# Kernel optimization log

Measured on AMD Instinct MI355X. Metric: run time of the kernel, lower is better.

Reference implementation:

```python
import jax, jax.numpy as jnp
import numpy as np


def setup_inputs() -> dict:
    key = jax.random.key(0)
    kx, ke = jax.random.split(key)
    B, D, H, W, K = 64, 64, 32, 32, 512
    x = jax.random.normal(kx, (B, D, H, W), dtype=jnp.float32)
    # matches nn.init.normal_(weight, mean=0.0, std=2*D**-0.5)
    emb = jax.random.normal(ke, (D, K), dtype=jnp.float32) * (2.0 * D ** -0.5)
    return {"x": x, "emb": emb}


def reference(x, emb):
    # x: (B, D, *spatial), emb: (D, K)
    B, D = x.shape[0], x.shape[1]
    spatial = x.shape[2:]
    xf = jnp.moveaxis(x, 1, -1).reshape(B, -1, D)  # (B, N, D)
    scores = -2.0 * jnp.einsum('bnd,dk->bnk', xf, emb) + jnp.sum(emb * emb, axis=0)  # (B, N, K)
    argmin = jnp.argmin(scores, axis=-1)  # (B, N) int
    quant = jnp.take(emb.T, argmin, axis=0)  # (B, N, D) gather from codebook
    result = jnp.moveaxis(quant.reshape(B, *spatial, D), -1, 1)  # (B, D, *spatial)
    return result, argmin.reshape(B, *spatial)
```

## Files before the change

### kernel.cpp

```cpp
#include <hip/hip_runtime.h>


constexpr int D    = 64;
constexpr int K    = 512;
constexpr int HW   = 1024;
constexpr int ROWS = 128;
constexpr int CK   = 128;
constexpr int NCH  = K / CK;

__device__ __forceinline__ void gload16(const float* g, float* l) {
    __builtin_amdgcn_global_load_lds(
        (const __attribute__((address_space(1))) void*)g,
        (__attribute__((address_space(3))) void*)l,
        16, 0, 0);
}

__global__ __launch_bounds__(256, 2) void vq_kernel(
    const float* __restrict__ x,
    const float* __restrict__ emb,
    float* __restrict__ out_q,
    float* __restrict__ out_idx)
{
    __shared__ float xs[D][ROWS];
    __shared__ float es[D][CK];
    __shared__ float e2s[K];
    __shared__ int   kfin[ROWS];

    const int tid = threadIdx.x;
    const int ct  = tid & 15;
    const int rg  = tid >> 4;
    const int r0  = blockIdx.x * ROWS;
    const int b   = r0 >> 10;
    const int n0  = r0 & (HW - 1);

    const float* xg = x + ((size_t)b * D) * HW + n0;

    #pragma unroll
    for (int p = 0; p < 8; ++p) {
        const int li = p * 256 + tid;
        const int d  = li >> 5;
        const int r4 = (li & 31) << 2;
        gload16(xg + (size_t)d * HW + r4, &xs[d][r4]);
    }

    #pragma unroll
    for (int h = 0; h < 2; ++h) {
        const int k = h * 256 + tid;
        float s = 0.f;
        #pragma unroll
        for (int d = 0; d < D; ++d) {
            const float v = emb[d * K + k];
            s = fmaf(v, v, s);
        }
        e2s[k] = s;
    }

    float best[8];
    int   bidx[8];
    #pragma unroll
    for (int j = 0; j < 8; ++j) { best[j] = 3.4e38f; bidx[j] = 0; }

    #pragma unroll 1
    for (int ch = 0; ch < NCH; ++ch) {
        __syncthreads();

        #pragma unroll
        for (int p = 0; p < 8; ++p) {
            const int li = p * 256 + tid;
            const int d  = li >> 5;
            const int c4 = (li & 31) << 2;
            gload16(emb + d * K + ch * CK + c4, &es[d][c4]);
        }
        __syncthreads();

        float acc[8][8];
        #pragma unroll
        for (int j = 0; j < 8; ++j)
            #pragma unroll
            for (int i = 0; i < 8; ++i) acc[j][i] = 0.f;

        #pragma unroll
        for (int d = 0; d < D; ++d) {
            const float4 xv0 = *reinterpret_cast<const float4*>(&xs[d][rg << 2]);
            const float4 xv1 = *reinterpret_cast<const float4*>(&xs[d][64 + (rg << 2)]);
            const float4 ev0 = *reinterpret_cast<const float4*>(&es[d][ct << 2]);
            const float4 ev1 = *reinterpret_cast<const float4*>(&es[d][64 + (ct << 2)]);
            const float* xa = reinterpret_cast<const float*>(&xv0);
            const float* xb = reinterpret_cast<const float*>(&xv1);
            const float* ea = reinterpret_cast<const float*>(&ev0);
            const float* eb = reinterpret_cast<const float*>(&ev1);
            #pragma unroll
            for (int j = 0; j < 4; ++j) {
                const float x0 = xa[j];
                const float x1 = xb[j];
                #pragma unroll
                for (int i = 0; i < 4; ++i) {
                    acc[j][i]         = fmaf(x0, ea[i], acc[j][i]);
                    acc[j][i + 4]     = fmaf(x0, eb[i], acc[j][i + 4]);
                    acc[j + 4][i]     = fmaf(x1, ea[i], acc[j + 4][i]);
                    acc[j + 4][i + 4] = fmaf(x1, eb[i], acc[j + 4][i + 4]);
                }
            }
        }

        const int kb = ch * CK;
        const float4 q0 = *reinterpret_cast<const float4*>(&e2s[kb + (ct << 2)]);
        const float4 q1 = *reinterpret_cast<const float4*>(&e2s[kb + 64 + (ct << 2)]);
        const float* qa = reinterpret_cast<const float*>(&q0);
        const float* qb = reinterpret_cast<const float*>(&q1);
        #pragma unroll
        for (int j = 0; j < 8; ++j) {
            #pragma unroll
            for (int i = 0; i < 4; ++i) {
                const float s0 = fmaf(-2.f, acc[j][i], qa[i]);
                if (s0 < best[j]) { best[j] = s0; bidx[j] = kb + (ct << 2) + i; }
            }
            #pragma unroll
            for (int i = 0; i < 4; ++i) {
                const float s1 = fmaf(-2.f, acc[j][i + 4], qb[i]);
                if (s1 < best[j]) { best[j] = s1; bidx[j] = kb + 64 + (ct << 2) + i; }
            }
        }
    }

    #pragma unroll
    for (int m = 1; m < 16; m <<= 1) {
        #pragma unroll
        for (int j = 0; j < 8; ++j) {
            const float ob = __shfl_xor(best[j], m, 64);
            const int   oi = __shfl_xor(bidx[j], m, 64);
            if (ob < best[j] || (ob == best[j] && oi < bidx[j])) {
                best[j] = ob; bidx[j] = oi;
            }
        }
    }

    if (ct == 0) {
        #pragma unroll
        for (int j = 0; j < 8; ++j) {
            const int rloc = (j < 4) ? ((rg << 2) + j) : (64 + (rg << 2) + (j - 4));
            kfin[rloc] = bidx[j];
            __builtin_nontemporal_store((float)bidx[j], &out_idx[r0 + rloc]);
        }
    }
    __syncthreads();

    const int row = tid & 127;
    const int dg  = tid >> 7;
    const int kq  = kfin[row];
    float* oq = out_q + ((size_t)b * D) * HW + n0 + row;
    #pragma unroll
    for (int j = 0; j < 32; ++j) {
        const int d = (dg << 5) + j;
        __builtin_nontemporal_store(emb[d * K + kq], &oq[(size_t)d * HW]);
    }
}

extern "C" void kernel_launch(void* const* d_in, const int* in_sizes, int n_in,
                              void* d_out, int out_size, void* d_ws, size_t ws_size,
                              hipStream_t stream)
{
    const float* x   = (const float*)d_in[0];
    const float* emb = (const float*)d_in[1];

    float* out_q   = (float*)d_out;
    float* out_idx = out_q + (size_t)64 * 64 * 1024;

    vq_kernel<<<512, 256, 0, stream>>>(x, emb, out_q, out_idx);
}
```

Baseline: 121.3 us.

## Enlarge row and codebook tiles to 256 with 512-thread blocks

```diff
diff --git a/kernel.cpp b/kernel.cpp
--- a/kernel.cpp
+++ b/kernel.cpp
@@ -4,8 +4,8 @@
 constexpr int D    = 64;
 constexpr int K    = 512;
 constexpr int HW   = 1024;
-constexpr int ROWS = 128;
-constexpr int CK   = 128;
+constexpr int ROWS = 256;
+constexpr int CK   = 256;
 constexpr int NCH  = K / CK;
 
 __device__ __forceinline__ void gload16(const float* g, float* l) {
@@ -15,7 +15,7 @@
         16, 0, 0);
 }
 
-__global__ __launch_bounds__(256, 2) void vq_kernel(
+__global__ __launch_bounds__(512, 1) void vq_kernel(
     const float* __restrict__ x,
     const float* __restrict__ emb,
     float* __restrict__ out_q,
@@ -37,88 +37,96 @@
 
     #pragma unroll
     for (int p = 0; p < 8; ++p) {
-        const int li = p * 256 + tid;
-        const int d  = li >> 5;
-        const int r4 = (li & 31) << 2;
+        const int li = p * 512 + tid;
+        const int d  = li >> 6;
+        const int r4 = (li & 63) << 2;
         gload16(xg + (size_t)d * HW + r4, &xs[d][r4]);
     }
+    #pragma unroll
+    for (int p = 0; p < 8; ++p) {
+        const int li = p * 512 + tid;
+        const int d  = li >> 6;
+        const int c4 = (li & 63) << 2;
+        gload16(emb + d * K + c4, &es[d][c4]);
+    }
 
-    #pragma unroll
-    for (int h = 0; h < 2; ++h) {
-        const int k = h * 256 + tid;
+    {
         float s = 0.f;
         #pragma unroll
         for (int d = 0; d < D; ++d) {
-            const float v = emb[d * K + k];
+            const float v = emb[d * K + tid];
             s = fmaf(v, v, s);
         }
-        e2s[k] = s;
+        e2s[tid] = s;
     }
 
     float best[8];
     int   bidx[8];
     #pragma unroll
-    for (int j = 0; j < 8; ++j) { best[j] = 3.4e38f; bidx[j] = 0; }
+    for (int r = 0; r < 8; ++r) { best[r] = 3.4e38f; bidx[r] = 0; }
 
-    #pragma unroll 1
+    #pragma unroll
     for (int ch = 0; ch < NCH; ++ch) {
-        __syncthreads();
-
-        #pragma unroll
-        for (int p = 0; p < 8; ++p) {
-            const int li = p * 256 + tid;
-            const int d  = li >> 5;
-            const int c4 = (li & 31) << 2;
-            gload16(emb + d * K + ch * CK + c4, &es[d][c4]);
+        if (ch > 0) {
+            __syncthreads();
+            #pragma unroll
+            for (int p = 0; p < 8; ++p) {
+                const int li = p * 512 + tid;
+                const int d  = li >> 6;
+                const int c4 = (li & 63) << 2;
+                gload16(emb + d * K + ch * CK + c4, &es[d][c4]);
+            }
         }
         __syncthreads();
 
-        float acc[8][8];
+        float acc[8][16];
         #pragma unroll
-        for (int j = 0; j < 8; ++j)
+        for (int r = 0; r < 8; ++r)
             #pragma unroll
-            for (int i = 0; i < 8; ++i) acc[j][i] = 0.f;
+            for (int c = 0; c < 16; ++c) acc[r][c] = 0.f;
 
-        #pragma unroll
+        #pragma unroll 2
         for (int d = 0; d < D; ++d) {
             const float4 xv0 = *reinterpret_cast<const float4*>(&xs[d][rg << 2]);
-            const float4 xv1 = *reinterpret_cast<const float4*>(&xs[d][64 + (rg << 2)]);
-            const float4 ev0 = *reinterpret_cast<const float4*>(&es[d][ct << 2]);
-            const float4 ev1 = *reinterpret_cast<const float4*>(&es[d][64 + (ct << 2)]);
+            const float4 xv1 = *reinterpret_cast<const float4*>(&xs[d][128 + (rg << 2)]);
+            float4 ev[4];
+            #pragma unroll
+            for (int j = 0; j < 4; ++j)
+                ev[j] = *reinterpret_cast<const float4*>(&es[d][(ct << 2) + 64 * j]);
             const float* xa = reinterpret_cast<const float*>(&xv0);
             const float* xb = reinterpret_cast<const float*>(&xv1);
-            const float* ea = reinterpret_cast<const float*>(&ev0);
-            const float* eb = reinterpret_cast<const float*>(&ev1);
             #pragma unroll
-            for (int j = 0; j < 4; ++j) {
-                const float x0 = xa[j];
-                const float x1 = xb[j];
+            for (int r = 0; r < 4; ++r) {
+                const float x0 = xa[r];
+                const float x1 = xb[r];
                 #pragma unroll
-                for (int i = 0; i < 4; ++i) {
-                    acc[j][i]         = fmaf(x0, ea[i], acc[j][i]);
-                    acc[j][i + 4]     = fmaf(x0, eb[i], acc[j][i + 4]);
-                    acc[j + 4][i]     = fmaf(x1, ea[i], acc[j + 4][i]);
-                    acc[j + 4][i + 4] = fmaf(x1, eb[i], acc[j + 4][i + 4]);
+                for (int j = 0; j < 4; ++j) {
+                    const float* ef = reinterpret_cast<const float*>(&ev[j]);
+                    #pragma unroll
+                    for (int i = 0; i < 4; ++i) {
+                        acc[r][j * 4 + i]     = fmaf(x0, ef[i], acc[r][j * 4 + i]);
+                        acc[r + 4][j * 4 + i] = fmaf(x1, ef[i], acc[r + 4][j * 4 + i]);
+                    }
                 }
             }
         }
 
         const int kb = ch * CK;
-        const float4 q0 = *reinterpret_cast<const float4*>(&e2s[kb + (ct << 2)]);
-        const float4 q1 = *reinterpret_cast<const float4*>(&e2s[kb + 64 + (ct << 2)]);
-        const float* qa = reinterpret_cast<const float*>(&q0);
-        const float* qb = reinterpret_cast<const float*>(&q1);
+        float4 q[4];
         #pragma unroll
-        for (int j = 0; j < 8; ++j) {
+        for (int j = 0; j < 4; ++j)
+            q[j] = *reinterpret_cast<const float4*>(&e2s[kb + (ct << 2) + 64 * j]);
+        #pragma unroll
+        for (int r = 0; r < 8; ++r) {
             #pragma unroll
-            for (int i = 0; i < 4; ++i) {
-                const float s0 = fmaf(-2.f, acc[j][i], qa[i]);
-                if (s0 < best[j]) { best[j] = s0; bidx[j] = kb + (ct << 2) + i; }
-            }
-            #pragma unroll
-            for (int i = 0; i < 4; ++i) {
-                const float s1 = fmaf(-2.f, acc[j][i + 4], qb[i]);
-                if (s1 < best[j]) { best[j] = s1; bidx[j] = kb + 64 + (ct << 2) + i; }
+            for (int j = 0; j < 4; ++j) {
+                const float* qf = reinterpret_cast<const float*>(&q[j]);
+                #pragma unroll
+                for (int i = 0; i < 4; ++i) {
+                    const float s = fmaf(-2.f, acc[r][j * 4 + i], qf[i]);
+                    const int   k = kb + 64 * j + (ct << 2) + i;
+                    if (s < best[r]) { best[r] = s; bidx[r] = k; }
+                }
             }
         }
     }
@@ -126,27 +134,27 @@
     #pragma unroll
     for (int m = 1; m < 16; m <<= 1) {
         #pragma unroll
-        for (int j = 0; j < 8; ++j) {
-            const float ob = __shfl_xor(best[j], m, 64);
-            const int   oi = __shfl_xor(bidx[j], m, 64);
-            if (ob < best[j] || (ob == best[j] && oi < bidx[j])) {
-                best[j] = ob; bidx[j] = oi;
+        for (int r = 0; r < 8; ++r) {
+            const float ob = __shfl_xor(best[r], m, 64);
+            const int   oi = __shfl_xor(bidx[r], m, 64);
+            if (ob < best[r] || (ob == best[r] && oi < bidx[r])) {
+                best[r] = ob; bidx[r] = oi;
             }
         }
     }
 
     if (ct == 0) {
         #pragma unroll
-        for (int j = 0; j < 8; ++j) {
-            const int rloc = (j < 4) ? ((rg << 2) + j) : (64 + (rg << 2) + (j - 4));
-            kfin[rloc] = bidx[j];
-            __builtin_nontemporal_store((float)bidx[j], &out_idx[r0 + rloc]);
+        for (int r = 0; r < 8; ++r) {
+            const int rloc = (r < 4) ? ((rg << 2) + r) : (128 + (rg << 2) + (r - 4));
+            kfin[rloc] = bidx[r];
+            __builtin_nontemporal_store((float)bidx[r], &out_idx[r0 + rloc]);
         }
     }
     __syncthreads();
 
-    const int row = tid & 127;
-    const int dg  = tid >> 7;
+    const int row = tid & 255;
+    const int dg  = tid >> 8;
     const int kq  = kfin[row];
     float* oq = out_q + ((size_t)b * D) * HW + n0 + row;
     #pragma unroll
@@ -166,5 +174,5 @@
     float* out_q   = (float*)d_out;
     float* out_idx = out_q + (size_t)64 * 64 * 1024;
 
-    vq_kernel<<<512, 256, 0, stream>>>(x, emb, out_q, out_idx);
+    vq_kernel<<<256, 512, 0, stream>>>(x, emb, out_q, out_idx);
 }
```

Result: slower. 137.9 us (+13.7%).
